# Kernel tuning notes

Measured on AMD Instinct MI355X. Metric: run time of the kernel, lower is better.

The kernel has to match this reference:

```python
import jax, jax.numpy as jnp
import numpy as np


def _bilinear_resize_nchw(x, out_h, out_w):
    """Torch F.interpolate(mode='bilinear', align_corners=False), no antialias."""
    B, C, H, W = x.shape

    def coords(out_n, in_n):
        src = jnp.maximum(0.0, (jnp.arange(out_n, dtype=jnp.float32) + 0.5) * (in_n / out_n) - 0.5)
        f = jnp.floor(src)
        i0 = jnp.clip(f.astype(jnp.int32), 0, in_n - 1)
        i1 = jnp.clip(i0 + 1, 0, in_n - 1)
        frac = src - f
        return i0, i1, frac

    y0, y1, fy = coords(out_h, H)
    x0, x1, fx = coords(out_w, W)
    rows = x[:, :, y0, :] * (1.0 - fy)[None, None, :, None] + x[:, :, y1, :] * fy[None, None, :, None]
    out = rows[:, :, :, x0] * (1.0 - fx)[None, None, None, :] + rows[:, :, :, x1] * fx[None, None, None, :]
    return out


def setup_inputs() -> dict:
    key = jax.random.key(0)
    k1, k2, k3, k4 = jax.random.split(key, 4)
    return {
        "query_value": jax.random.normal(k1, (2, 256, 64, 128), dtype=jnp.float32),
        "memory_keys_low": jax.random.normal(k2, (2, 4, 64, 32, 64), dtype=jnp.float32),
        "memory_values_low": jax.random.normal(k3, (2, 4, 256, 32, 64), dtype=jnp.float32),
        "query_key_low": jax.random.normal(k4, (2, 64, 32, 64), dtype=jnp.float32),
    }


def reference(query_value, memory_keys_low, memory_values_low, query_key_low):
    B, T, Ck, H, W = memory_keys_low.shape
    Cv = memory_values_low.shape[2]
    # keys: BxTxCkxHxW -> Bx(T*H*W)xCk via permute(0,2,1,3,4)+view+permute
    mk = jnp.transpose(memory_keys_low, (0, 2, 1, 3, 4)).reshape(B, Ck, T * H * W)
    qk = query_key_low.reshape(B, Ck, H * W)
    # attn[b, m, n] over memory locations m (softmax axis), query locations n
    attn = jnp.einsum('bcm,bcn->bmn', mk, qk)  # [B, T*H*W, H*W]
    # matmul_norm=False: no key_channels**-0.5 scaling
    attn = jax.nn.softmax(attn, axis=1)
    mv = jnp.transpose(memory_values_low, (0, 2, 1, 3, 4)).reshape(B, Cv, T * H * W)
    memory = jnp.einsum('bcm,bmn->bcn', mv, attn).reshape(B, Cv, H, W)
    qv = _bilinear_resize_nchw(query_value, H, W)
    return jnp.concatenate([qv, memory], axis=1)  # [B, 2*Cv, H, W]
```

## Files before the change

### kernel.cpp

```cpp
#include <hip/hip_runtime.h>
#include <cstdint>

#define BATCH 2
#define TT    4
#define CKD   64
#define CVD   256
#define NQ    2048
#define MM    8192
#define TQ    64
#define TM    32
#define MSPLIT 8
#define MCHUNK (MM / MSPLIT)
#define NIT    (MCHUNK / TM)

typedef unsigned short u16;
typedef __bf16 bf16x8 __attribute__((ext_vector_type(8)));
typedef float  f32x4  __attribute__((ext_vector_type(4)));

struct __attribute__((aligned(8)))  U16x4 { u16 x, y, z, w; };
struct __attribute__((aligned(16))) U16x8 { u16 v[8]; };

__device__ __forceinline__ u16 f2bf(float x) {
    uint32_t u = __float_as_uint(x);
    uint32_t r = (u + 0x7FFFu + ((u >> 16) & 1u)) >> 16;
    return (u16)r;
}
__device__ __forceinline__ float bf2f(u16 h) {
    return __uint_as_float(((uint32_t)h) << 16);
}

#define MFMA(a, b, c) __builtin_amdgcn_mfma_f32_16x16x32_bf16((a), (b), (c), 0, 0, 0)

#define WS_VB   0u
#define WS_KHI  8388608u
#define WS_KLO  10485760u
#define WS_QHI  12582912u
#define WS_QLO  13107200u
#define WS_LP   13631488u
#define WS_UP   13762560u

__global__ __launch_bounds__(256) void prep_v(const float* __restrict__ mv,
                                              u16* __restrict__ vb) {
    int idx = blockIdx.x * 256 + threadIdx.x;
    const float4* s = (const float4*)mv + (size_t)idx * 2;
    float4 a = s[0], b = s[1];
    U16x8 o;
    o.v[0] = f2bf(a.x); o.v[1] = f2bf(a.y); o.v[2] = f2bf(a.z); o.v[3] = f2bf(a.w);
    o.v[4] = f2bf(b.x); o.v[5] = f2bf(b.y); o.v[6] = f2bf(b.z); o.v[7] = f2bf(b.w);
    *(U16x8*)(vb + (size_t)idx * 8) = o;
}

__global__ __launch_bounds__(256) void prep_kq(const float* __restrict__ src,
                                               u16* __restrict__ dhi,
                                               u16* __restrict__ dlo) {
    int g  = blockIdx.x >> 6;
    int mg = blockIdx.x & 63;
    int c8 = (threadIdx.x & 7) * 8;
    int m  = mg * 32 + (threadIdx.x >> 3);
    const float* s = src + (size_t)g * 64 * 2048 + m;
    U16x8 hi, lo;
    #pragma unroll
    for (int j = 0; j < 8; ++j) {
        float v = s[(size_t)(c8 + j) * 2048];
        u16 h = f2bf(v);
        hi.v[j] = h;
        lo.v[j] = f2bf(v - bf2f(h));
    }
    size_t o = ((size_t)g * 2048 + m) * 64 + c8;
    *(U16x8*)(dhi + o) = hi;
    *(U16x8*)(dlo + o) = lo;
}

__global__ __launch_bounds__(256) void pool_qv(const float* __restrict__ qv,
                                               float* __restrict__ out) {
    int idx = blockIdx.x * 256 + threadIdx.x;
    int n  = idx & 2047;
    int bc = idx >> 11;
    int x = n & 63, y = n >> 6;
    const float* ib = qv + (size_t)bc * (64 * 128) + (2 * y) * 128 + 2 * x;
    float2 r0 = *(const float2*)ib;
    float2 r1 = *(const float2*)(ib + 128);
    int b = bc >> 8, c = bc & 255;
    out[((size_t)(b * 512 + c)) * NQ + n] = 0.25f * (r0.x + r0.y + r1.x + r1.y);
}

__global__ __launch_bounds__(256, 2)
void flash_attn(const u16* __restrict__ khi_g, const u16* __restrict__ klo_g,
                const u16* __restrict__ vb_g, const u16* __restrict__ qhi_g,
                const u16* __restrict__ qlo_g, float* __restrict__ Up,
                float* __restrict__ Lp) {
    __shared__ __align__(16) u16 smem[17408];
    u16* Khi = smem;
    u16* Klo = smem + 2304;
    u16* Vs  = smem + 4608;
    u16* Ps  = smem + 14848;

    const int tid    = threadIdx.x;
    const int bx     = blockIdx.x;
    const int mchunk = bx & 7;
    const int ntile  = (bx >> 3) & 31;
    const int b      = bx >> 8;

    const int lane = tid & 63;
    const int w    = tid >> 6;
    const int quad = lane >> 4;
    const int l15  = lane & 15;

    const int bt      = b * TT + (mchunk >> 1);
    const int hw_base = (mchunk & 1) * MCHUNK;

    bf16x8 qh[2][2], ql[2][2];
    {
        const int nbase = ntile * TQ + (w >> 1) * 32;
        #pragma unroll
        for (int nsi = 0; nsi < 2; ++nsi) {
            size_t o = ((size_t)(b * NQ + nbase + nsi * 16 + l15)) * 64 + quad * 8;
            qh[nsi][0] = *(const bf16x8*)&qhi_g[o];
            qh[nsi][1] = *(const bf16x8*)&qhi_g[o + 32];
            ql[nsi][0] = *(const bf16x8*)&qlo_g[o];
            ql[nsi][1] = *(const bf16x8*)&qlo_g[o + 32];
        }
    }

    const u16* kh_base = khi_g + ((size_t)bt * 2048 + hw_base) * 64;
    const u16* kl_base = klo_g + ((size_t)bt * 2048 + hw_base) * 64;
    const u16* v_base  = vb_g + (size_t)bt * CVD * 2048 + hw_base;

    f32x4 O[2][8];
    #pragma unroll
    for (int i = 0; i < 2; ++i)
        #pragma unroll
        for (int j = 0; j < 8; ++j)
            O[i][j] = (f32x4){0.f, 0.f, 0.f, 0.f};
    float Lloc[2] = {0.f, 0.f};

    const int msub     = w & 1;
    const int nsubpair = w >> 1;
    const int npair    = w & 1;
    const int chalf    = w >> 1;

    const int km = tid >> 3;
    const int kc = (tid & 7) * 8;
    const int vc = tid >> 2;
    const int vm = (tid & 3) * 8;

    bf16x8 kh_r = *(const bf16x8*)&kh_base[(size_t)km * 64 + kc];
    bf16x8 kl_r = *(const bf16x8*)&kl_base[(size_t)km * 64 + kc];
    bf16x8 v_r[4];
    #pragma unroll
    for (int p = 0; p < 4; ++p)
        v_r[p] = *(const bf16x8*)&v_base[(size_t)(vc + p * 64) * 2048 + vm];

    for (int it = 0; it < NIT; ++it) {
        *(bf16x8*)&Khi[km * 72 + kc] = kh_r;
        *(bf16x8*)&Klo[km * 72 + kc] = kl_r;
        #pragma unroll
        for (int p = 0; p < 4; ++p)
            *(bf16x8*)&Vs[(vc + p * 64) * 40 + vm] = v_r[p];
        __syncthreads();

        if (it + 1 < NIT) {
            const int hw1 = (it + 1) * TM;
            kh_r = *(const bf16x8*)&kh_base[(size_t)(hw1 + km) * 64 + kc];
            kl_r = *(const bf16x8*)&kl_base[(size_t)(hw1 + km) * 64 + kc];
            #pragma unroll
            for (int p = 0; p < 4; ++p)
                v_r[p] = *(const bf16x8*)&v_base[(size_t)(vc + p * 64) * 2048 + hw1 + vm];
        }

        f32x4 acc[2];
        acc[0] = (f32x4){0.f, 0.f, 0.f, 0.f};
        acc[1] = (f32x4){0.f, 0.f, 0.f, 0.f};
        #pragma unroll
        for (int ks = 0; ks < 2; ++ks) {
            bf16x8 ah = *(const bf16x8*)&Khi[(msub * 16 + l15) * 72 + ks * 32 + quad * 8];
            bf16x8 al = *(const bf16x8*)&Klo[(msub * 16 + l15) * 72 + ks * 32 + quad * 8];
            #pragma unroll
            for (int nsi = 0; nsi < 2; ++nsi) {
                acc[nsi] = MFMA(ah, qh[nsi][ks], acc[nsi]);
                acc[nsi] = MFMA(ah, ql[nsi][ks], acc[nsi]);
                acc[nsi] = MFMA(al, qh[nsi][ks], acc[nsi]);
            }
        }
        #pragma unroll
        for (int nsi = 0; nsi < 2; ++nsi) {
            int n = (nsubpair * 2 + nsi) * 16 + l15;
            float p0 = __expf(acc[nsi][0]);
            float p1 = __expf(acc[nsi][1]);
            float p2 = __expf(acc[nsi][2]);
            float p3 = __expf(acc[nsi][3]);
            Lloc[nsi] += (p0 + p1) + (p2 + p3);
            U16x4 pk = {f2bf(p0), f2bf(p1), f2bf(p2), f2bf(p3)};
            *(U16x4*)&Ps[n * 40 + msub * 16 + quad * 4] = pk;
        }
        __syncthreads();

        bf16x8 a2[2];
        #pragma unroll
        for (int nsi2 = 0; nsi2 < 2; ++nsi2)
            a2[nsi2] = *(const bf16x8*)&Ps[(npair * 32 + nsi2 * 16 + l15) * 40 + quad * 8];
        #pragma unroll
        for (int cs = 0; cs < 8; ++cs) {
            bf16x8 bv = *(const bf16x8*)&Vs[(chalf * 128 + cs * 16 + l15) * 40 + quad * 8];
            O[0][cs] = MFMA(a2[0], bv, O[0][cs]);
            O[1][cs] = MFMA(a2[1], bv, O[1][cs]);
        }
        __syncthreads();
    }

    #pragma unroll
    for (int nsi = 0; nsi < 2; ++nsi) {
        float v = Lloc[nsi];
        v += __shfl_xor(v, 16);
        v += __shfl_xor(v, 32);
        if (quad == nsi) {
            int nsub = nsubpair * 2 + nsi;
            atomicAdd(&Lp[((size_t)mchunk * BATCH + b) * NQ + ntile * TQ + nsub * 16 + l15], v);
        }
    }

    float* ubase = Up + (((size_t)mchunk * BATCH + b) * NQ + ntile * TQ) * CVD
                 + (size_t)(npair * 32) * CVD + chalf * 128;
    #pragma unroll
    for (int nsi2 = 0; nsi2 < 2; ++nsi2) {
        #pragma unroll
        for (int cs = 0; cs < 8; ++cs) {
            #pragma unroll
            for (int r = 0; r < 4; ++r) {
                int n_local = nsi2 * 16 + quad * 4 + r;
                ubase[(size_t)n_local * CVD + cs * 16 + l15] = O[nsi2][cs][r];
            }
        }
    }
}

__global__ __launch_bounds__(256) void reduce_div(const float* __restrict__ Up,
                                                  const float* __restrict__ Lp,
                                                  float* __restrict__ out) {
    __shared__ float lds[16 * 257];
    const int tid = threadIdx.x;
    const int b   = blockIdx.x >> 7;
    const int n0  = (blockIdx.x & 127) * 16;

    float acc[16];
    #pragma unroll
    for (int j = 0; j < 16; ++j) acc[j] = 0.f;

    for (int ms = 0; ms < MSPLIT; ++ms) {
        const float* sb = Up + (((size_t)ms * BATCH + b) * NQ + n0) * CVD + tid * 16;
        #pragma unroll
        for (int k = 0; k < 4; ++k) {
            float4 v = *(const float4*)(sb + k * 4);
            acc[k * 4 + 0] += v.x; acc[k * 4 + 1] += v.y;
            acc[k * 4 + 2] += v.z; acc[k * 4 + 3] += v.w;
        }
    }

    const int n_local = tid >> 4;
    const int c0      = (tid & 15) * 16;
    float Lsum = 0.f;
    for (int ms = 0; ms < MSPLIT; ++ms)
        Lsum += Lp[((size_t)ms * BATCH + b) * NQ + n0 + n_local];
    const float inv = 1.0f / Lsum;

    #pragma unroll
    for (int j = 0; j < 16; ++j)
        lds[n_local * 257 + c0 + j] = acc[j] * inv;
    __syncthreads();

    float* ob = out + ((size_t)(b * 512 + 256 + tid)) * NQ + n0;
    #pragma unroll
    for (int k = 0; k < 4; ++k) {
        float4 v;
        v.x = lds[(4 * k + 0) * 257 + tid];
        v.y = lds[(4 * k + 1) * 257 + tid];
        v.z = lds[(4 * k + 2) * 257 + tid];
        v.w = lds[(4 * k + 3) * 257 + tid];
        *(float4*)(ob + 4 * k) = v;
    }
}

extern "C" void kernel_launch(void* const* d_in, const int* in_sizes, int n_in,
                              void* d_out, int out_size, void* d_ws, size_t ws_size,
                              hipStream_t stream) {
    const float* qv = (const float*)d_in[0];
    const float* mk = (const float*)d_in[1];
    const float* mv = (const float*)d_in[2];
    const float* qk = (const float*)d_in[3];
    float* out = (float*)d_out;

    u16*   vb  = (u16*)((char*)d_ws + WS_VB);
    u16*   khi = (u16*)((char*)d_ws + WS_KHI);
    u16*   klo = (u16*)((char*)d_ws + WS_KLO);
    u16*   qhi = (u16*)((char*)d_ws + WS_QHI);
    u16*   qlo = (u16*)((char*)d_ws + WS_QLO);
    float* Lp  = (float*)((char*)d_ws + WS_LP);
    float* Up  = (float*)((char*)d_ws + WS_UP);

    hipMemsetAsync(Lp, 0, (size_t)MSPLIT * BATCH * NQ * sizeof(float), stream);

    prep_v<<<2048, 256, 0, stream>>>(mv, vb);
    prep_kq<<<512, 256, 0, stream>>>(mk, khi, klo);
    prep_kq<<<128, 256, 0, stream>>>(qk, qhi, qlo);
    pool_qv<<<4096, 256, 0, stream>>>(qv, out);
    flash_attn<<<512, 256, 0, stream>>>(khi, klo, vb, qhi, qlo, Up, Lp);
    reduce_div<<<256, 256, 0, stream>>>(Up, Lp, out);
}
```

Baseline: 146.1 us.

## Fuse prep kernels, double-buffer LDS in flash loop, drop memset and atomics

Merges the four preprocessing kernels into one launch, which removes the memset as well as several launch gaps. The flash_attn loop now double-buffers its shared memory so one barrier per iteration can be dropped, and the next tile's global loads are issued before that barrier. Row-sum partials are written per msub slot and summed in reduce_div instead of being atomically accumulated into zeroed memory. Doubling LDS to about 68KB per block may reduce occupancy below the two blocks per CU the launch bounds target.

```diff
diff --git a/kernel.cpp b/kernel.cpp
--- a/kernel.cpp
+++ b/kernel.cpp
@@ -37,51 +37,58 @@
 #define WS_QHI  12582912u
 #define WS_QLO  13107200u
 #define WS_LP   13631488u
-#define WS_UP   13762560u
-
-__global__ __launch_bounds__(256) void prep_v(const float* __restrict__ mv,
-                                              u16* __restrict__ vb) {
-    int idx = blockIdx.x * 256 + threadIdx.x;
-    const float4* s = (const float4*)mv + (size_t)idx * 2;
-    float4 a = s[0], b = s[1];
-    U16x8 o;
-    o.v[0] = f2bf(a.x); o.v[1] = f2bf(a.y); o.v[2] = f2bf(a.z); o.v[3] = f2bf(a.w);
-    o.v[4] = f2bf(b.x); o.v[5] = f2bf(b.y); o.v[6] = f2bf(b.z); o.v[7] = f2bf(b.w);
-    *(U16x8*)(vb + (size_t)idx * 8) = o;
-}
-
-__global__ __launch_bounds__(256) void prep_kq(const float* __restrict__ src,
-                                               u16* __restrict__ dhi,
-                                               u16* __restrict__ dlo) {
-    int g  = blockIdx.x >> 6;
-    int mg = blockIdx.x & 63;
-    int c8 = (threadIdx.x & 7) * 8;
-    int m  = mg * 32 + (threadIdx.x >> 3);
-    const float* s = src + (size_t)g * 64 * 2048 + m;
-    U16x8 hi, lo;
-    #pragma unroll
-    for (int j = 0; j < 8; ++j) {
-        float v = s[(size_t)(c8 + j) * 2048];
-        u16 h = f2bf(v);
-        hi.v[j] = h;
-        lo.v[j] = f2bf(v - bf2f(h));
-    }
-    size_t o = ((size_t)g * 2048 + m) * 64 + c8;
-    *(U16x8*)(dhi + o) = hi;
-    *(U16x8*)(dlo + o) = lo;
-}
-
-__global__ __launch_bounds__(256) void pool_qv(const float* __restrict__ qv,
-                                               float* __restrict__ out) {
-    int idx = blockIdx.x * 256 + threadIdx.x;
-    int n  = idx & 2047;
-    int bc = idx >> 11;
-    int x = n & 63, y = n >> 6;
-    const float* ib = qv + (size_t)bc * (64 * 128) + (2 * y) * 128 + 2 * x;
-    float2 r0 = *(const float2*)ib;
-    float2 r1 = *(const float2*)(ib + 128);
-    int b = bc >> 8, c = bc & 255;
-    out[((size_t)(b * 512 + c)) * NQ + n] = 0.25f * (r0.x + r0.y + r1.x + r1.y);
+#define WS_UP   13893632u
+
+__global__ __launch_bounds__(256)
+void prep_fused(const float* __restrict__ qv, const float* __restrict__ mk,
+                const float* __restrict__ qk, const float* __restrict__ mv,
+                float* __restrict__ out, u16* __restrict__ vb,
+                u16* __restrict__ khi, u16* __restrict__ klo,
+                u16* __restrict__ qhi, u16* __restrict__ qlo) {
+    const int bid = blockIdx.x;
+    const int tid = threadIdx.x;
+
+    if (bid < 4096) {
+        int idx = bid * 256 + tid;
+        int n  = idx & 2047;
+        int bc = idx >> 11;
+        int x = n & 63, y = n >> 6;
+        const float* ib = qv + (size_t)bc * (64 * 128) + (2 * y) * 128 + 2 * x;
+        float2 r0 = *(const float2*)ib;
+        float2 r1 = *(const float2*)(ib + 128);
+        int b = bc >> 8, c = bc & 255;
+        out[((size_t)(b * 512 + c)) * NQ + n] = 0.25f * (r0.x + r0.y + r1.x + r1.y);
+    } else if (bid < 6144) {
+        int idx = (bid - 4096) * 256 + tid;
+        const float4* s = (const float4*)mv + (size_t)idx * 2;
+        float4 a = s[0], b = s[1];
+        U16x8 o;
+        o.v[0] = f2bf(a.x); o.v[1] = f2bf(a.y); o.v[2] = f2bf(a.z); o.v[3] = f2bf(a.w);
+        o.v[4] = f2bf(b.x); o.v[5] = f2bf(b.y); o.v[6] = f2bf(b.z); o.v[7] = f2bf(b.w);
+        *(U16x8*)(vb + (size_t)idx * 8) = o;
+    } else {
+        const float* src;
+        u16 *dhi, *dlo;
+        int blk;
+        if (bid < 6656) { src = mk; dhi = khi; dlo = klo; blk = bid - 6144; }
+        else            { src = qk; dhi = qhi; dlo = qlo; blk = bid - 6656; }
+        int g  = blk >> 6;
+        int mg = blk & 63;
+        int c8 = (tid & 7) * 8;
+        int m  = mg * 32 + (tid >> 3);
+        const float* s = src + (size_t)g * 64 * 2048 + m;
+        U16x8 hi, lo;
+        #pragma unroll
+        for (int j = 0; j < 8; ++j) {
+            float v = s[(size_t)(c8 + j) * 2048];
+            u16 h = f2bf(v);
+            hi.v[j] = h;
+            lo.v[j] = f2bf(v - bf2f(h));
+        }
+        size_t o = ((size_t)g * 2048 + m) * 64 + c8;
+        *(U16x8*)(dhi + o) = hi;
+        *(U16x8*)(dlo + o) = lo;
+    }
 }
 
 __global__ __launch_bounds__(256, 2)
@@ -89,11 +96,7 @@
                 const u16* __restrict__ vb_g, const u16* __restrict__ qhi_g,
                 const u16* __restrict__ qlo_g, float* __restrict__ Up,
                 float* __restrict__ Lp) {
-    __shared__ __align__(16) u16 smem[17408];
-    u16* Khi = smem;
-    u16* Klo = smem + 2304;
-    u16* Vs  = smem + 4608;
-    u16* Ps  = smem + 14848;
+    __shared__ __align__(16) u16 smem[2][17408];
 
     const int tid    = threadIdx.x;
     const int bx     = blockIdx.x;
@@ -151,13 +154,18 @@
     for (int p = 0; p < 4; ++p)
         v_r[p] = *(const bf16x8*)&v_base[(size_t)(vc + p * 64) * 2048 + vm];
 
+    #pragma unroll 2
     for (int it = 0; it < NIT; ++it) {
+        u16* Khi = smem[it & 1];
+        u16* Klo = Khi + 2304;
+        u16* Vs  = Khi + 4608;
+        u16* Ps  = Khi + 14848;
+
         *(bf16x8*)&Khi[km * 72 + kc] = kh_r;
         *(bf16x8*)&Klo[km * 72 + kc] = kl_r;
         #pragma unroll
         for (int p = 0; p < 4; ++p)
             *(bf16x8*)&Vs[(vc + p * 64) * 40 + vm] = v_r[p];
-        __syncthreads();
 
         if (it + 1 < NIT) {
             const int hw1 = (it + 1) * TM;
@@ -167,6 +175,7 @@
             for (int p = 0; p < 4; ++p)
                 v_r[p] = *(const bf16x8*)&v_base[(size_t)(vc + p * 64) * 2048 + hw1 + vm];
         }
+        __syncthreads();
 
         f32x4 acc[2];
         acc[0] = (f32x4){0.f, 0.f, 0.f, 0.f};
@@ -205,7 +214,6 @@
             O[0][cs] = MFMA(a2[0], bv, O[0][cs]);
             O[1][cs] = MFMA(a2[1], bv, O[1][cs]);
         }
-        __syncthreads();
     }
 
     #pragma unroll
@@ -215,7 +223,7 @@
         v += __shfl_xor(v, 32);
         if (quad == nsi) {
             int nsub = nsubpair * 2 + nsi;
-            atomicAdd(&Lp[((size_t)mchunk * BATCH + b) * NQ + ntile * TQ + nsub * 16 + l15], v);
+            Lp[(((size_t)mchunk * 2 + msub) * BATCH + b) * NQ + ntile * TQ + nsub * 16 + l15] = v;
         }
     }
 
@@ -259,8 +267,9 @@
     const int n_local = tid >> 4;
     const int c0      = (tid & 15) * 16;
     float Lsum = 0.f;
-    for (int ms = 0; ms < MSPLIT; ++ms)
-        Lsum += Lp[((size_t)ms * BATCH + b) * NQ + n0 + n_local];
+    #pragma unroll
+    for (int s = 0; s < MSPLIT * 2; ++s)
+        Lsum += Lp[((size_t)s * BATCH + b) * NQ + n0 + n_local];
     const float inv = 1.0f / Lsum;
 
     #pragma unroll
@@ -297,12 +306,7 @@
     float* Lp  = (float*)((char*)d_ws + WS_LP);
     float* Up  = (float*)((char*)d_ws + WS_UP);
 
-    hipMemsetAsync(Lp, 0, (size_t)MSPLIT * BATCH * NQ * sizeof(float), stream);
-
-    prep_v<<<2048, 256, 0, stream>>>(mv, vb);
-    prep_kq<<<512, 256, 0, stream>>>(mk, khi, klo);
-    prep_kq<<<128, 256, 0, stream>>>(qk, qhi, qlo);
-    pool_qv<<<4096, 256, 0, stream>>>(qv, out);
+    prep_fused<<<6784, 256, 0, stream>>>(qv, mk, qk, mv, out, vb, khi, klo, qhi, qlo);
     flash_attn<<<512, 256, 0, stream>>>(khi, klo, vb, qhi, qlo, Up, Lp);
     reduce_div<<<256, 256, 0, stream>>>(Up, Lp, out);
 }
```

Result: faster. 138.1 us (-5.5%).
